# Kernel optimization log

Hardware: AMD Instinct MI355X
Metric: run time of the kernel (lower is better)

Reference implementation:

```python
import jax, jax.numpy as jnp
import numpy as np

B, L, D, H = 2, 2048, 2048, 16
C = D // H  # head dim = 128
EPS = 1e-5


def setup_inputs() -> dict:
    key = jax.random.key(0)
    k1, k2, k3, k4 = jax.random.split(key, 4)
    scale = 1.0 / np.sqrt(D)
    return {
        "x": jax.random.normal(k1, (B, L, D), dtype=jnp.float32),
        "theta": jax.random.uniform(k2, (B, L, D // 2), dtype=jnp.float32) * 6.2831853,
        "w_qkv": jax.random.normal(k3, (3 * D, D), dtype=jnp.float32) * scale,
        "w_y": jax.random.normal(k4, (D, D), dtype=jnp.float32) * scale,
        "b_y": jnp.zeros((D,), dtype=jnp.float32),
    }


def _rms_norm(t):
    # RMSNorm over last dim, eps=1e-5, no affine
    return t * jax.lax.rsqrt(jnp.mean(t * t, axis=-1, keepdims=True) + EPS)


def _apply_rope(q, k, theta):
    # q, k: (B, H, L, C); theta: (B, H, L, C//2)
    qr, qi = q[..., 0::2], q[..., 1::2]
    kr, ki = k[..., 0::2], k[..., 1::2]
    cos_t, sin_t = jnp.cos(theta), jnp.sin(theta)
    q_rot = jnp.stack((qr * cos_t - qi * sin_t, qr * sin_t + qi * cos_t), axis=-1).reshape(q.shape)
    k_rot = jnp.stack((kr * cos_t - ki * sin_t, kr * sin_t + ki * cos_t), axis=-1).reshape(k.shape)
    return q_rot, k_rot


def reference(x, theta, w_qkv, w_y, b_y):
    # QKV projection: (B, L, 3D)
    qkv = jnp.einsum("bld,ed->ble", x, w_qkv)
    # rearrange '... L (n H C) -> n ... H L C'
    qkv = qkv.reshape(B, L, 3, H, C).transpose(2, 0, 3, 1, 4)  # (3, B, H, L, C)
    q, k, v = qkv[0], qkv[1], qkv[2]
    q, k = _rms_norm(q), _rms_norm(k)
    # theta: (B, L, H*C/2) -> (B, H, L, C/2)
    th = theta.reshape(B, L, H, C // 2).transpose(0, 2, 1, 3)
    q, k = _apply_rope(q, k, th)
    # scaled dot-product attention
    scores = jnp.einsum("bhqc,bhkc->bhqk", q, k) / np.sqrt(C).astype(np.float32)
    attn = jax.nn.softmax(scores, axis=-1)
    y = jnp.einsum("bhqk,bhkc->bhqc", attn, v)
    # (B, H, L, C) -> (B, L, H*C)
    y = y.transpose(0, 2, 1, 3).reshape(B, L, D)
    return jnp.einsum("bld,ed->ble", y, w_y) + b_y
```

## Files before the change

### kernel.cpp

```cpp
#include <hip/hip_runtime.h>
#include <stdint.h>

typedef uint16_t u16;
typedef __attribute__((ext_vector_type(8))) short bf16x8;
typedef __attribute__((ext_vector_type(4))) float f32x4;


__device__ __forceinline__ u16 f2bf(float f) {
  uint32_t u = __builtin_bit_cast(uint32_t, f);
  u += 0x7fffu + ((u >> 16) & 1u);
  return (u16)(u >> 16);
}
__device__ __forceinline__ float bf2f(u16 h) {
  return __builtin_bit_cast(float, (uint32_t)h << 16);
}
__device__ __forceinline__ uint32_t pack2bf(float a, float b) {
  uint32_t ua = __builtin_bit_cast(uint32_t, a) + 0x7fffu;
  uint32_t ub = __builtin_bit_cast(uint32_t, b) + 0x7fffu;
  return (ua >> 16) | (ub & 0xffff0000u);
}
__device__ __forceinline__ void gl_lds16(const u16* g, u16* l) {
  __builtin_amdgcn_global_load_lds((const __attribute__((address_space(1))) uint32_t*)g,
                                   (__attribute__((address_space(3))) uint32_t*)l, 16, 0, 0);
}

__global__ __launch_bounds__(256) void castk(const float* __restrict__ in,
                                             u16* __restrict__ out, int n) {
  int idx = (blockIdx.x * 256 + threadIdx.x) * 4;
  int stride = gridDim.x * 256 * 4;
  for (int i = idx; i < n; i += stride) {
    float4 v = *(const float4*)(in + i);
    uint32_t lo = (uint32_t)f2bf(v.x) | ((uint32_t)f2bf(v.y) << 16);
    uint32_t hi = (uint32_t)f2bf(v.z) | ((uint32_t)f2bf(v.w) << 16);
    *(uint2*)(out + i) = make_uint2(lo, hi);
  }
}

__global__ __launch_bounds__(512, 1) void gemm8_qkv(
    const u16* __restrict__ A, const u16* __restrict__ Bw,
    u16* __restrict__ qb, u16* __restrict__ kb, u16* __restrict__ vt) {
  __shared__ u16 sm[57344];
  const int K = 2048;
  const int tid = threadIdx.x, lane = tid & 63;
  const int wid = tid >> 6, g = lane >> 4, lr = lane & 15;
  const int wm = wid >> 2, wn = wid & 3;
  const int m0 = blockIdx.y * 256, n0 = blockIdx.x * 192;
  const int srow = tid >> 3, sjs = (tid & 7) ^ (srow & 7);

  auto stA = [&](int buf, int kt, int R) {
    gl_lds16(A + (size_t)(m0 + R + srow) * K + kt * 64 + sjs * 8,
             &sm[buf * 28672 + R * 64 + tid * 8]);
  };
  auto stB = [&](int buf, int kt, int R) {
    gl_lds16(Bw + (size_t)(n0 + R + srow) * K + kt * 64 + sjs * 8,
             &sm[buf * 28672 + 16384 + R * 64 + tid * 8]);
  };
  auto rdA = [&](const u16* As, int mf, int ks) {
    int ra = wm * 128 + mf * 16 + lr;
    return *(const bf16x8*)&As[ra * 64 + (((ks * 4 + g) ^ (ra & 7)) * 8)];
  };
  auto rdB = [&](const u16* Bs, int nf, int ks) {
    int rb = wn * 48 + nf * 16 + lr;
    return *(const bf16x8*)&Bs[rb * 64 + (((ks * 4 + g) ^ (rb & 7)) * 8)];
  };

  f32x4 acc[8][3] = {};
  bf16x8 bc[3][2], bn[3][2], afc[2][2], afn[2][2];

  stB(0, 0, 0); stB(0, 0, 64); stB(0, 0, 128);
  stA(0, 0, 0); stA(0, 0, 128);
  stA(0, 0, 64); stA(0, 0, 192);
  asm volatile("s_waitcnt vmcnt(2)" ::: "memory");
  __builtin_amdgcn_s_barrier();
  {
    const u16* As0 = &sm[0];
    const u16* Bs0 = &sm[16384];
#pragma unroll
    for (int nf = 0; nf < 3; ++nf)
#pragma unroll
      for (int ks = 0; ks < 2; ++ks) bc[nf][ks] = rdB(Bs0, nf, ks);
#pragma unroll
    for (int i = 0; i < 2; ++i)
#pragma unroll
      for (int ks = 0; ks < 2; ++ks) afn[i][ks] = rdA(As0, i, ks);
  }

  for (int t = 0; t < 32; ++t) {
    const int cur = t & 1, nxt = cur ^ 1;
    const int kn = (t < 31) ? t + 1 : 31;
    const u16* Asc = &sm[cur * 28672];
    const u16* Asn = &sm[nxt * 28672];
    const u16* Bsn = &sm[nxt * 28672 + 16384];

#pragma unroll
    for (int p = 0; p < 4; ++p) {
#pragma unroll
      for (int i = 0; i < 2; ++i)
#pragma unroll
        for (int ks = 0; ks < 2; ++ks) afc[i][ks] = afn[i][ks];
      if (p == 0) {
        stB(nxt, kn, 0); stB(nxt, kn, 64); stB(nxt, kn, 128);
        asm volatile("s_waitcnt vmcnt(3)" ::: "memory");
      } else if (p == 1) {
        stA(nxt, kn, 0); stA(nxt, kn, 128);
      } else if (p == 2) {
        stA(nxt, kn, 64); stA(nxt, kn, 192);
      } else {
        asm volatile("s_waitcnt vmcnt(2)" ::: "memory");
      }
      __builtin_amdgcn_s_barrier();
      if (p < 3) {
#pragma unroll
        for (int i = 0; i < 2; ++i)
#pragma unroll
          for (int ks = 0; ks < 2; ++ks) afn[i][ks] = rdA(Asc, (p + 1) * 2 + i, ks);
      } else {
#pragma unroll
        for (int nf = 0; nf < 3; ++nf)
#pragma unroll
          for (int ks = 0; ks < 2; ++ks) bn[nf][ks] = rdB(Bsn, nf, ks);
#pragma unroll
        for (int i = 0; i < 2; ++i)
#pragma unroll
          for (int ks = 0; ks < 2; ++ks) afn[i][ks] = rdA(Asn, i, ks);
      }
      __builtin_amdgcn_s_setprio(1);
#pragma unroll
      for (int i = 0; i < 2; ++i)
#pragma unroll
        for (int nf = 0; nf < 3; ++nf) {
          acc[p * 2 + i][nf] = __builtin_amdgcn_mfma_f32_16x16x32_bf16(
              afc[i][0], bc[nf][0], acc[p * 2 + i][nf], 0, 0, 0);
          acc[p * 2 + i][nf] = __builtin_amdgcn_mfma_f32_16x16x32_bf16(
              afc[i][1], bc[nf][1], acc[p * 2 + i][nf], 0, 0, 0);
        }
      __builtin_amdgcn_s_setprio(0);
    }
#pragma unroll
    for (int nf = 0; nf < 3; ++nf)
#pragma unroll
      for (int ks = 0; ks < 2; ++ks) bc[nf][ks] = bn[nf][ks];
  }
  asm volatile("s_waitcnt vmcnt(0)" ::: "memory");

#pragma unroll
  for (int mf = 0; mf < 8; ++mf)
#pragma unroll
    for (int nf = 0; nf < 3; ++nf) {
      int n = n0 + wn * 48 + nf * 16 + lr;
      int s = n >> 11, h = (n >> 7) & 15, cb = n & 127;
#pragma unroll
      for (int r = 0; r < 4; ++r) {
        int m = m0 + wm * 128 + mf * 16 + g * 4 + r;
        int b = m >> 11, lp = m & 2047;
        u16 val = f2bf(acc[mf][nf][r]);
        if (s == 0)
          qb[(size_t)((b * 16 + h) * 2048 + lp) * 128 + cb] = val;
        else if (s == 1)
          kb[(size_t)((b * 16 + h) * 2048 + lp) * 128 + cb] = val;
        else
          vt[(size_t)((b * 16 + h) * 128 + cb) * 2048 + lp] = val;
      }
    }
}

__global__ __launch_bounds__(256) void gemm_out(
    const u16* __restrict__ A, const u16* __restrict__ Bw, int K,
    float* __restrict__ out, const float* __restrict__ bias) {
  __shared__ u16 As[128 * 64];
  __shared__ u16 Bs[128 * 64];
  const int tid = threadIdx.x;
  const int lane = tid & 63, wid = tid >> 6;
  const int g = lane >> 4, lr = lane & 15;
  const int wm = wid >> 1, wn = wid & 1;
  const int m0 = blockIdx.y * 128, n0 = blockIdx.x * 128;
  f32x4 acc[4][4] = {};
  const int nk = K >> 6;
  for (int kt = 0; kt < nk; ++kt) {
    const int kbase = kt * 64;
#pragma unroll
    for (int i = 0; i < 4; ++i) {
      int ci = wid * 256 + i * 64 + lane;
      int row = ci >> 3, j = ci & 7;
      int js = j ^ (row & 7);
      gl_lds16(A + (size_t)(m0 + row) * K + kbase + js * 8, &As[(wid * 256 + i * 64) * 8]);
    }
#pragma unroll
    for (int i = 0; i < 4; ++i) {
      int ci = wid * 256 + i * 64 + lane;
      int row = ci >> 3, j = ci & 7;
      int js = j ^ (row & 7);
      gl_lds16(Bw + (size_t)(n0 + row) * K + kbase + js * 8, &Bs[(wid * 256 + i * 64) * 8]);
    }
    __syncthreads();
#pragma unroll
    for (int ks = 0; ks < 2; ++ks) {
      bf16x8 af[4], bfr[4];
#pragma unroll
      for (int t = 0; t < 4; ++t) {
        int ra = wm * 64 + t * 16 + lr;
        af[t] = *(const bf16x8*)&As[ra * 64 + (((ks * 4 + g) ^ (ra & 7)) * 8)];
        int rb = wn * 64 + t * 16 + lr;
        bfr[t] = *(const bf16x8*)&Bs[rb * 64 + (((ks * 4 + g) ^ (rb & 7)) * 8)];
      }
#pragma unroll
      for (int mt = 0; mt < 4; ++mt)
#pragma unroll
        for (int nt = 0; nt < 4; ++nt)
          acc[mt][nt] =
              __builtin_amdgcn_mfma_f32_16x16x32_bf16(af[mt], bfr[nt], acc[mt][nt], 0, 0, 0);
    }
    __syncthreads();
  }
#pragma unroll
  for (int mt = 0; mt < 4; ++mt)
#pragma unroll
    for (int nt = 0; nt < 4; ++nt) {
      int n = n0 + wn * 64 + nt * 16 + lr;
      float bv = bias[n];
#pragma unroll
      for (int r = 0; r < 4; ++r) {
        int m = m0 + wm * 64 + mt * 16 + g * 4 + r;
        out[(size_t)m * 2048 + n] = acc[mt][nt][r] + bv;
      }
    }
}

__global__ __launch_bounds__(256) void qk_fix(u16* __restrict__ qb, u16* __restrict__ kb,
                                              const float* __restrict__ theta) {
  const int row = blockIdx.x * 4 + (threadIdx.x >> 6);
  const int lane = threadIdx.x & 63;
  const int bh = row >> 11, l = row & 2047;
  const int b = bh >> 4, h = bh & 15;
  float th = theta[(size_t)(b * 2048 + l) * 1024 + h * 64 + lane];
  float sn, cs;
  __sincosf(th, &sn, &cs);
#pragma unroll
  for (int which = 0; which < 2; ++which) {
    u16* buf = which ? kb : qb;
    uint32_t* p = (uint32_t*)(buf + (size_t)row * 128) + lane;
    uint32_t v = *p;
    float x0 = bf2f((u16)(v & 0xffff)), x1 = bf2f((u16)(v >> 16));
    float ss = x0 * x0 + x1 * x1;
#pragma unroll
    for (int m = 1; m <= 32; m <<= 1) ss += __shfl_xor(ss, m);
    float rn = rsqrtf(ss * (1.0f / 128.0f) + 1e-5f);
    if (which == 0) rn *= 0.12751743f;
    x0 *= rn;
    x1 *= rn;
    float y0 = x0 * cs - x1 * sn;
    float y1 = x0 * sn + x1 * cs;
    *p = (uint32_t)f2bf(y0) | ((uint32_t)f2bf(y1) << 16);
  }
}

__global__ __launch_bounds__(256, 2) void attn_k(const u16* __restrict__ qb,
                                                 const u16* __restrict__ kb,
                                                 const u16* __restrict__ vt,
                                                 u16* __restrict__ yb) {
  __shared__ u16 sm[32768];
  const int gid = blockIdx.x;
  const int slot = gid & 7, rest = gid >> 3;
  const int bh = slot * 4 + (rest & 3);
  const int qtile = rest >> 2;
  const int b = bh >> 4, h = bh & 15;
  const int tid = threadIdx.x, lane = tid & 63, wid = tid >> 6;
  const int g = lane >> 4, lr = lane & 15;
  const int q0 = qtile * 128 + wid * 32;

  bf16x8 qf[2][4];
#pragma unroll
  for (int qs = 0; qs < 2; ++qs) {
    const u16* qrow = qb + (size_t)(bh * 2048 + q0 + qs * 16 + lr) * 128;
#pragma unroll
    for (int ks = 0; ks < 4; ++ks) qf[qs][ks] = *(const bf16x8*)&qrow[ks * 32 + g * 8];
  }

  auto stage = [&](int buf, int kv) {
#pragma unroll
    for (int i = 0; i < 2; ++i) {
      int ci = i * 256 + tid;
      int row = ci >> 4, j = ci & 15;
      gl_lds16(kb + (size_t)(bh * 2048 + kv + row) * 128 + (j ^ (row & 7)) * 8,
               &sm[buf * 8192 + ci * 8]);
    }
#pragma unroll
    for (int i = 2; i < 4; ++i) {
      int ci = (i - 2) * 256 + tid;
      int row = ci >> 4, j = ci & 15;
      gl_lds16(kb + (size_t)(bh * 2048 + kv + 32 + row) * 128 + (j ^ (row & 7)) * 8,
               &sm[buf * 8192 + 4096 + ci * 8]);
    }
#pragma unroll
    for (int i = 0; i < 4; ++i) {
      int ci = i * 256 + tid;
      int row = ci >> 3, j = ci & 7;
      gl_lds16(vt + (size_t)(bh * 128 + row) * 2048 + kv + (j ^ (row & 7)) * 8,
               &sm[16384 + buf * 8192 + ci * 8]);
    }
  };

  f32x4 acc[2][8] = {};
  float mrun[2] = {-1e30f, -1e30f}, lrun[2] = {0.f, 0.f};
  const int sA = (2 * (g & 1)) * 16 + lr, sB = sA + 16;
  const bool hi2 = (g >> 1) != 0;

  stage(0, 0);
  asm volatile("s_waitcnt vmcnt(0)" ::: "memory");
  __builtin_amdgcn_s_barrier();

  for (int t = 0; t < 32; ++t) {
    const int cur = t & 1;
    if (t < 31) stage(cur ^ 1, (t + 1) * 64);
    const u16* Ks = &sm[cur * 8192];
    const u16* Vs = &sm[16384 + cur * 8192];

    f32x4 st[2][4] = {};
#pragma unroll
    for (int ks = 0; ks < 4; ++ks) {
      bf16x8 kf[4];
#pragma unroll
      for (int kt = 0; kt < 4; ++kt) {
        int row = kt * 16 + lr;
        kf[kt] = *(const bf16x8*)&Ks[row * 128 + (((ks * 4 + g) ^ (row & 7)) * 8)];
      }
#pragma unroll
      for (int kt = 0; kt < 4; ++kt)
#pragma unroll
        for (int qs = 0; qs < 2; ++qs)
          st[qs][kt] =
              __builtin_amdgcn_mfma_f32_16x16x32_bf16(kf[kt], qf[qs][ks], st[qs][kt], 0, 0, 0);
    }

    float pmax[2];
#pragma unroll
    for (int qs = 0; qs < 2; ++qs) {
      float mx = st[qs][0][0];
#pragma unroll
      for (int kt = 0; kt < 4; ++kt)
#pragma unroll
        for (int r = 0; r < 4; ++r) mx = fmaxf(mx, st[qs][kt][r]);
      mx = fmaxf(mx, __shfl_xor(mx, 16));
      mx = fmaxf(mx, __shfl_xor(mx, 32));
      pmax[qs] = mx;
    }
    float need = fmaxf(pmax[0] - mrun[0], pmax[1] - mrun[1]);
    if (!__all(need <= 8.0f)) {
#pragma unroll
      for (int qs = 0; qs < 2; ++qs) {
        float mnew = fmaxf(mrun[qs], pmax[qs]);
        float corr = __builtin_amdgcn_exp2f(mrun[qs] - mnew);
        lrun[qs] *= corr;
        mrun[qs] = mnew;
#pragma unroll
        for (int ct = 0; ct < 8; ++ct) {
          acc[qs][ct][0] *= corr;
          acc[qs][ct][1] *= corr;
          acc[qs][ct][2] *= corr;
          acc[qs][ct][3] *= corr;
        }
      }
    }
    uint32_t pw[2][4][2];
#pragma unroll
    for (int qs = 0; qs < 2; ++qs) {
      float rsum = 0.f;
#pragma unroll
      for (int kt = 0; kt < 4; ++kt)
#pragma unroll
        for (int hf = 0; hf < 2; ++hf) {
          float e0 = __builtin_amdgcn_exp2f(st[qs][kt][2 * hf] - mrun[qs]);
          float e1 = __builtin_amdgcn_exp2f(st[qs][kt][2 * hf + 1] - mrun[qs]);
          rsum += e0 + e1;
          pw[qs][kt][hf] = pack2bf(e0, e1);
        }
      rsum += __shfl_xor(rsum, 16);
      rsum += __shfl_xor(rsum, 32);
      lrun[qs] += rsum;
    }

#pragma unroll
    for (int ks2 = 0; ks2 < 2; ++ks2) {
      bf16x8 pf[2];
#pragma unroll
      for (int qs = 0; qs < 2; ++qs) {
        uint32_t a0 = __shfl(pw[qs][ks2 * 2][0], sA);
        uint32_t a1 = __shfl(pw[qs][ks2 * 2][1], sA);
        uint32_t a2 = __shfl(pw[qs][ks2 * 2][0], sB);
        uint32_t a3 = __shfl(pw[qs][ks2 * 2][1], sB);
        uint32_t b0 = __shfl(pw[qs][ks2 * 2 + 1][0], sA);
        uint32_t b1 = __shfl(pw[qs][ks2 * 2 + 1][1], sA);
        uint32_t b2 = __shfl(pw[qs][ks2 * 2 + 1][0], sB);
        uint32_t b3 = __shfl(pw[qs][ks2 * 2 + 1][1], sB);
        union {
          uint32_t u[4];
          bf16x8 v;
        } tt;
        tt.u[0] = hi2 ? b0 : a0;
        tt.u[1] = hi2 ? b1 : a1;
        tt.u[2] = hi2 ? b2 : a2;
        tt.u[3] = hi2 ? b3 : a3;
        pf[qs] = tt.v;
      }
#pragma unroll
      for (int ct = 0; ct < 8; ++ct) {
        int row = ct * 16 + lr;
        bf16x8 vf = *(const bf16x8*)&Vs[row * 64 + (((ks2 * 4 + g) ^ (row & 7)) * 8)];
#pragma unroll
        for (int qs = 0; qs < 2; ++qs)
          acc[qs][ct] = __builtin_amdgcn_mfma_f32_16x16x32_bf16(vf, pf[qs], acc[qs][ct], 0, 0, 0);
      }
    }
    if (t < 31) {
      asm volatile("s_waitcnt vmcnt(0)" ::: "memory");
      __builtin_amdgcn_s_barrier();
    }
  }

#pragma unroll
  for (int qs = 0; qs < 2; ++qs) {
    float inv = 1.f / lrun[qs];
    const size_t orow = (size_t)(b * 2048 + q0 + qs * 16 + lr) * 2048 + h * 128;
#pragma unroll
    for (int ct = 0; ct < 8; ++ct) {
      uint32_t lo = pack2bf(acc[qs][ct][0] * inv, acc[qs][ct][1] * inv);
      uint32_t hi = pack2bf(acc[qs][ct][2] * inv, acc[qs][ct][3] * inv);
      *(uint2*)&yb[orow + ct * 16 + g * 4] = make_uint2(lo, hi);
    }
  }
}

extern "C" void kernel_launch(void* const* d_in, const int* in_sizes, int n_in,
                              void* d_out, int out_size, void* d_ws, size_t ws_size,
                              hipStream_t stream) {
  const float* x = (const float*)d_in[0];
  const float* theta = (const float*)d_in[1];
  const float* wqkv = (const float*)d_in[2];
  const float* wy = (const float*)d_in[3];
  const float* by = (const float*)d_in[4];
  float* out = (float*)d_out;
  char* ws = (char*)d_ws;
  u16* xb  = (u16*)(ws + 0);
  u16* wqb = (u16*)(ws + 16777216);
  u16* wyb = (u16*)(ws + 41943040);
  u16* qb  = (u16*)(ws + 50331648);
  u16* kb  = (u16*)(ws + 67108864);
  u16* vt  = (u16*)(ws + 83886080);
  u16* yb  = (u16*)(ws + 100663296);

  castk<<<2048, 256, 0, stream>>>(x, xb, 2 * 2048 * 2048);
  castk<<<2048, 256, 0, stream>>>(wqkv, wqb, 3 * 2048 * 2048);
  castk<<<1024, 256, 0, stream>>>(wy, wyb, 2048 * 2048);

  gemm8_qkv<<<dim3(32, 16), 512, 0, stream>>>(xb, wqb, qb, kb, vt);
  qk_fix<<<16384, 256, 0, stream>>>(qb, kb, theta);
  attn_k<<<512, 256, 0, stream>>>(qb, kb, vt, yb);
  gemm_out<<<dim3(16, 32), 256, 0, stream>>>(yb, wyb, 2048, out, by);
}
```

Before: 303.2 us.

## Restructure GEMM k-loop into two half-phases with fewer barriers

Rewrites the QKV GEMM main loop so that each k-tile runs in two phases of 4 M-fragments each, with one barrier per phase, replacing the four-phase schedule with a barrier in every phase. B fragments are now read from the current buffer at the start of each tile instead of being prefetched from the next buffer. The aim is to cut barrier and wait overhead and give larger MFMA batches between syncs. In exchange, LDS read latency is exposed more at each phase start, and register pressure rises from the larger fragment arrays.

```diff
diff --git a/kernel.cpp b/kernel.cpp
--- a/kernel.cpp
+++ b/kernel.cpp
@@ -65,7 +65,7 @@
   };
 
   f32x4 acc[8][3] = {};
-  bf16x8 bc[3][2], bn[3][2], afc[2][2], afn[2][2];
+  bf16x8 bc[3][2], fP0[4][2], fP1[4][2];
 
   stB(0, 0, 0); stB(0, 0, 64); stB(0, 0, 128);
   stA(0, 0, 0); stA(0, 0, 128);
@@ -74,72 +74,61 @@
   __builtin_amdgcn_s_barrier();
   {
     const u16* As0 = &sm[0];
-    const u16* Bs0 = &sm[16384];
-#pragma unroll
-    for (int nf = 0; nf < 3; ++nf)
-#pragma unroll
-      for (int ks = 0; ks < 2; ++ks) bc[nf][ks] = rdB(Bs0, nf, ks);
-#pragma unroll
-    for (int i = 0; i < 2; ++i)
-#pragma unroll
-      for (int ks = 0; ks < 2; ++ks) afn[i][ks] = rdA(As0, i, ks);
+#pragma unroll
+    for (int i = 0; i < 4; ++i)
+#pragma unroll
+      for (int ks = 0; ks < 2; ++ks) fP0[i][ks] = rdA(As0, i, ks);
   }
 
   for (int t = 0; t < 32; ++t) {
     const int cur = t & 1, nxt = cur ^ 1;
     const int kn = (t < 31) ? t + 1 : 31;
     const u16* Asc = &sm[cur * 28672];
+    const u16* Bsc = &sm[cur * 28672 + 16384];
     const u16* Asn = &sm[nxt * 28672];
-    const u16* Bsn = &sm[nxt * 28672 + 16384];
-
-#pragma unroll
-    for (int p = 0; p < 4; ++p) {
-#pragma unroll
-      for (int i = 0; i < 2; ++i)
-#pragma unroll
-        for (int ks = 0; ks < 2; ++ks) afc[i][ks] = afn[i][ks];
-      if (p == 0) {
-        stB(nxt, kn, 0); stB(nxt, kn, 64); stB(nxt, kn, 128);
-        asm volatile("s_waitcnt vmcnt(3)" ::: "memory");
-      } else if (p == 1) {
-        stA(nxt, kn, 0); stA(nxt, kn, 128);
-      } else if (p == 2) {
-        stA(nxt, kn, 64); stA(nxt, kn, 192);
-      } else {
-        asm volatile("s_waitcnt vmcnt(2)" ::: "memory");
-      }
-      __builtin_amdgcn_s_barrier();
-      if (p < 3) {
-#pragma unroll
-        for (int i = 0; i < 2; ++i)
-#pragma unroll
-          for (int ks = 0; ks < 2; ++ks) afn[i][ks] = rdA(Asc, (p + 1) * 2 + i, ks);
-      } else {
-#pragma unroll
-        for (int nf = 0; nf < 3; ++nf)
-#pragma unroll
-          for (int ks = 0; ks < 2; ++ks) bn[nf][ks] = rdB(Bsn, nf, ks);
-#pragma unroll
-        for (int i = 0; i < 2; ++i)
-#pragma unroll
-          for (int ks = 0; ks < 2; ++ks) afn[i][ks] = rdA(Asn, i, ks);
-      }
-      __builtin_amdgcn_s_setprio(1);
-#pragma unroll
-      for (int i = 0; i < 2; ++i)
-#pragma unroll
-        for (int nf = 0; nf < 3; ++nf) {
-          acc[p * 2 + i][nf] = __builtin_amdgcn_mfma_f32_16x16x32_bf16(
-              afc[i][0], bc[nf][0], acc[p * 2 + i][nf], 0, 0, 0);
-          acc[p * 2 + i][nf] = __builtin_amdgcn_mfma_f32_16x16x32_bf16(
-              afc[i][1], bc[nf][1], acc[p * 2 + i][nf], 0, 0, 0);
-        }
-      __builtin_amdgcn_s_setprio(0);
-    }
+
+    stB(nxt, kn, 0); stB(nxt, kn, 64); stB(nxt, kn, 128);
+    stA(nxt, kn, 0); stA(nxt, kn, 128);
+    asm volatile("s_waitcnt vmcnt(5)" ::: "memory");
+    __builtin_amdgcn_s_barrier();
 #pragma unroll
     for (int nf = 0; nf < 3; ++nf)
 #pragma unroll
-      for (int ks = 0; ks < 2; ++ks) bc[nf][ks] = bn[nf][ks];
+      for (int ks = 0; ks < 2; ++ks) bc[nf][ks] = rdB(Bsc, nf, ks);
+#pragma unroll
+    for (int i = 0; i < 4; ++i)
+#pragma unroll
+      for (int ks = 0; ks < 2; ++ks) fP1[i][ks] = rdA(Asc, 4 + i, ks);
+    __builtin_amdgcn_s_setprio(1);
+#pragma unroll
+    for (int i = 0; i < 4; ++i)
+#pragma unroll
+      for (int nf = 0; nf < 3; ++nf) {
+        acc[i][nf] = __builtin_amdgcn_mfma_f32_16x16x32_bf16(
+            fP0[i][0], bc[nf][0], acc[i][nf], 0, 0, 0);
+        acc[i][nf] = __builtin_amdgcn_mfma_f32_16x16x32_bf16(
+            fP0[i][1], bc[nf][1], acc[i][nf], 0, 0, 0);
+      }
+    __builtin_amdgcn_s_setprio(0);
+
+    stA(nxt, kn, 64); stA(nxt, kn, 192);
+    asm volatile("s_waitcnt vmcnt(2)" ::: "memory");
+    __builtin_amdgcn_s_barrier();
+#pragma unroll
+    for (int i = 0; i < 4; ++i)
+#pragma unroll
+      for (int ks = 0; ks < 2; ++ks) fP0[i][ks] = rdA(Asn, i, ks);
+    __builtin_amdgcn_s_setprio(1);
+#pragma unroll
+    for (int i = 0; i < 4; ++i)
+#pragma unroll
+      for (int nf = 0; nf < 3; ++nf) {
+        acc[4 + i][nf] = __builtin_amdgcn_mfma_f32_16x16x32_bf16(
+            fP1[i][0], bc[nf][0], acc[4 + i][nf], 0, 0, 0);
+        acc[4 + i][nf] = __builtin_amdgcn_mfma_f32_16x16x32_bf16(
+            fP1[i][1], bc[nf][1], acc[4 + i][nf], 0, 0, 0);
+      }
+    __builtin_amdgcn_s_setprio(0);
   }
   asm volatile("s_waitcnt vmcnt(0)" ::: "memory");
 
```

After: 299.2 us. Within noise of the previous version (-1.3%).
